# Kernel optimization log

Hardware: AMD Instinct MI355X
Metric: run time of the kernel (lower is better)

Reference implementation:

```python
import jax, jax.numpy as jnp
import numpy as np

N_NODES = 50000
N_EDGES = 625000
HIDDEN = 128
N_TYPES = 4


def setup_inputs() -> dict:
    key = jax.random.key(0)
    ks = jax.random.split(key, 10)
    s = 1.0 / np.sqrt(HIDDEN)
    return {
        "node_states": jax.random.normal(ks[0], (N_NODES, HIDDEN), dtype=jnp.float32),
        "edge_index": jax.random.randint(ks[1], (2, N_EDGES), 0, N_NODES, dtype=jnp.int64),
        "edge_type": jax.random.randint(ks[2], (N_EDGES,), 0, N_TYPES, dtype=jnp.int64),
        # per-edge-type Linear(hidden, hidden): weight [T, d, d] (torch: y = x @ W.T + b)
        "edge_W": jax.random.uniform(ks[3], (N_TYPES, HIDDEN, HIDDEN), jnp.float32, -s, s),
        "edge_b": jax.random.uniform(ks[4], (N_TYPES, HIDDEN), jnp.float32, -s, s),
        # GRUCell params (torch layout: [3d, d] for r|z|n gates)
        "w_ih": jax.random.uniform(ks[5], (3 * HIDDEN, HIDDEN), jnp.float32, -s, s),
        "w_hh": jax.random.uniform(ks[6], (3 * HIDDEN, HIDDEN), jnp.float32, -s, s),
        "b_ih": jax.random.uniform(ks[7], (3 * HIDDEN,), jnp.float32, -s, s),
        "b_hh": jax.random.uniform(ks[8], (3 * HIDDEN,), jnp.float32, -s, s),
    }


def reference(node_states, edge_index, edge_type, edge_W, edge_b, w_ih, w_hh, b_ih, b_hh):
    num_nodes = node_states.shape[0]
    src, dst = edge_index[0], edge_index[1]
    x_src = node_states[src]  # [E, d] gather of source states

    # per-edge-type linear; small fixed loop over edge types, masked accumulate
    msgs = jnp.zeros_like(x_src)
    for t in range(edge_W.shape[0]):
        m_t = x_src @ edge_W[t].T + edge_b[t]  # [E, d]
        msgs = msgs + jnp.where((edge_type == t)[:, None], m_t, 0.0)

    # scatter-sum messages into destination nodes
    agg = jax.ops.segment_sum(msgs, dst, num_segments=num_nodes)  # [N, d]

    # GRUCell(agg, node_states) — torch semantics
    gi = agg @ w_ih.T + b_ih          # [N, 3d]
    gh = node_states @ w_hh.T + b_hh  # [N, 3d]
    i_r, i_z, i_n = jnp.split(gi, 3, axis=1)
    h_r, h_z, h_n = jnp.split(gh, 3, axis=1)
    r = jax.nn.sigmoid(i_r + h_r)
    z = jax.nn.sigmoid(i_z + h_z)
    n = jnp.tanh(i_n + r * h_n)
    return (1.0 - z) * n + z * node_states
```

## Files before the change

### kernel.cpp

```cpp
#include <hip/hip_runtime.h>


typedef __attribute__((ext_vector_type(8))) short short8;
typedef __attribute__((ext_vector_type(4))) float floatx4;

#define HID 128
#define NTY 4

__device__ __forceinline__ unsigned short f2bf(float f) {
    unsigned int u = __float_as_uint(f);
    unsigned int r = (u + 0x7fffu + ((u >> 16) & 1u)) >> 16;
    return (unsigned short)r;
}
__device__ __forceinline__ float bf2f(unsigned int lo16) {
    return __uint_as_float(lo16 << 16);
}
__device__ __forceinline__ float frcp(float x) { return __builtin_amdgcn_rcpf(x); }


__global__ void prep_kernel(const float* __restrict__ h, unsigned short* __restrict__ hbf,
                            const float* __restrict__ W, unsigned short* __restrict__ Wc,
                            const float* __restrict__ w_ih, const float* __restrict__ w_hh,
                            unsigned short* __restrict__ Wg, float* __restrict__ bias4,
                            const float* __restrict__ b_ih, const float* __restrict__ b_hh,
                            int* __restrict__ deg4, int total4, int nb_cvt, int N4) {
    int b = blockIdx.x, tt = threadIdx.x;
    if (b < nb_cvt) {
        int i = b * 256 + tt;
        if (i < total4) {
            float4 v = ((const float4*)h)[i];
            uint2 o;
            o.x = (unsigned int)f2bf(v.x) | ((unsigned int)f2bf(v.y) << 16);
            o.y = (unsigned int)f2bf(v.z) | ((unsigned int)f2bf(v.w) << 16);
            ((uint2*)hbf)[i] = o;
        }
    } else if (b < nb_cvt + 256) {
        int idx = (b - nb_cvt) * 256 + tt;
        int j = idx >> 9, rem = idx & 511;
        int t = rem >> 7, k = rem & 127;
        Wc[idx] = f2bf(W[(t * HID + j) * HID + k]);
    } else if (b < nb_cvt + 768) {
        int idx = (b - nb_cvt - 256) * 256 + tt;
        int row = idx >> 8, k = idx & 255;
        int j = row >> 2, g = row & 3;
        float v = 0.0f;
        if (g == 0) v = (k < 128) ? w_ih[j * 128 + k]         : w_hh[j * 128 + (k - 128)];
        else if (g == 1) v = (k < 128) ? w_ih[(128 + j) * 128 + k] : w_hh[(128 + j) * 128 + (k - 128)];
        else if (g == 2) v = (k < 128) ? w_ih[(256 + j) * 128 + k] : 0.0f;
        else             v = (k < 128) ? 0.0f : w_hh[(256 + j) * 128 + (k - 128)];
        Wg[idx] = f2bf(v);
    } else if (b == nb_cvt + 768) {
        if (tt < 128) {
            float4 v;
            v.x = b_ih[tt] + b_hh[tt];
            v.y = b_ih[128 + tt] + b_hh[128 + tt];
            v.z = b_ih[256 + tt];
            v.w = b_hh[256 + tt];
            ((float4*)bias4)[tt] = v;
        }
    } else {
        int i = (b - nb_cvt - 769) * 256 + tt;
        if (i < N4) deg4[i] = 0;
    }
}


__global__ void hist4_kernel(const int* __restrict__ dst, const int* __restrict__ ety,
                             int* __restrict__ deg4, int E) {
    int e = blockIdx.x * blockDim.x + threadIdx.x;
    if (e < E) atomicAdd(&deg4[dst[e] * 4 + ety[e]], 1);
}

__global__ void scan_blocks4_kernel(const int* __restrict__ deg, int* __restrict__ rowptr,
                                    int* __restrict__ blocksum, int N4) {
    __shared__ int s[256];
    int t = threadIdx.x;
    int base = blockIdx.x * 1024 + t * 4;
    int v0 = 0, v1 = 0, v2 = 0, v3 = 0;
    if (base + 3 < N4) {
        v0 = deg[base]; v1 = deg[base + 1]; v2 = deg[base + 2]; v3 = deg[base + 3];
    } else {
        if (base < N4) v0 = deg[base];
        if (base + 1 < N4) v1 = deg[base + 1];
        if (base + 2 < N4) v2 = deg[base + 2];
    }
    int sum = v0 + v1 + v2 + v3;
    s[t] = sum;
    __syncthreads();
#pragma unroll
    for (int off = 1; off < 256; off <<= 1) {
        int x = (t >= off) ? s[t - off] : 0;
        __syncthreads();
        s[t] += x;
        __syncthreads();
    }
    int ex = s[t] - sum;
    if (base < N4) rowptr[base] = ex;
    if (base + 1 < N4) rowptr[base + 1] = ex + v0;
    if (base + 2 < N4) rowptr[base + 2] = ex + v0 + v1;
    if (base + 3 < N4) rowptr[base + 3] = ex + v0 + v1 + v2;
    if (t == 255) blocksum[blockIdx.x] = s[255];
}

__global__ void scan_top_kernel(const int* __restrict__ blocksum, int* __restrict__ blockoff, int nb) {
    __shared__ int s[256];
    int t = threadIdx.x;
    int v = (t < nb) ? blocksum[t] : 0;
    s[t] = v;
    __syncthreads();
#pragma unroll
    for (int off = 1; off < 256; off <<= 1) {
        int x = (t >= off) ? s[t - off] : 0;
        __syncthreads();
        s[t] += x;
        __syncthreads();
    }
    if (t < nb) blockoff[t] = s[t] - v;
}

__global__ void finalize4_kernel(int* __restrict__ rowptr, const int* __restrict__ blockoff,
                                 int* __restrict__ cursor, int N4, int E) {
    int i = blockIdx.x * blockDim.x + threadIdx.x;
    if (i >= N4) return;
    int r = rowptr[i] + blockoff[i >> 10];
    rowptr[i] = r;
    cursor[i] = r;
    if (i == 0) rowptr[N4] = E;
}

__global__ void fill4_kernel(const int* __restrict__ src, const int* __restrict__ dst,
                             const int* __restrict__ ety, int* __restrict__ cursor,
                             int* __restrict__ csr, int E) {
    int e = blockIdx.x * blockDim.x + threadIdx.x;
    if (e >= E) return;
    int pos = atomicAdd(&cursor[dst[e] * 4 + ety[e]], 1);
    csr[pos] = src[e];
}


__global__ void gather_s_kernel(const int* __restrict__ rowptr4, const int* __restrict__ csr,
                                const unsigned int* __restrict__ hbu,
                                float4* __restrict__ cnt4, unsigned int* __restrict__ Su, int N) {
    int w = blockIdx.x * (blockDim.x >> 6) + (threadIdx.x >> 6);
    if (w >= N) return;
    int lane = threadIdx.x & 63;
    int b0 = __builtin_amdgcn_readfirstlane(rowptr4[w * 4]);
    int b1 = __builtin_amdgcn_readfirstlane(rowptr4[w * 4 + 1]);
    int b2 = __builtin_amdgcn_readfirstlane(rowptr4[w * 4 + 2]);
    int b3 = __builtin_amdgcn_readfirstlane(rowptr4[w * 4 + 3]);
    int b4 = __builtin_amdgcn_readfirstlane(rowptr4[w * 4 + 4]);

    float s0 = 0.f, s1 = 0.f;
    float sn0[3], sn1[3];

    int e = b0;
    while (e + 8 <= b4) {
        int p[8];
        unsigned int u[8];
#pragma unroll
        for (int i = 0; i < 8; ++i) p[i] = csr[e + i];
#pragma unroll
        for (int i = 0; i < 8; ++i) u[i] = hbu[(size_t)p[i] * 64 + lane];
#pragma unroll
        for (int i = 0; i < 8; ++i) {
            int idx = e + i;
            if (idx == b1) { sn0[0] = s0; sn1[0] = s1; }
            if (idx == b2) { sn0[1] = s0; sn1[1] = s1; }
            if (idx == b3) { sn0[2] = s0; sn1[2] = s1; }
            s0 += bf2f(u[i] & 0xffffu);
            s1 += bf2f(u[i] >> 16);
        }
        e += 8;
    }
    {
        int rem = b4 - e;
        int p[7];
        unsigned int u[7];
#pragma unroll
        for (int i = 0; i < 7; ++i) if (i < rem) p[i] = csr[e + i];
#pragma unroll
        for (int i = 0; i < 7; ++i) if (i < rem) u[i] = hbu[(size_t)p[i] * 64 + lane];
#pragma unroll
        for (int i = 0; i < 7; ++i) {
            if (i < rem) {
                int idx = e + i;
                if (idx == b1) { sn0[0] = s0; sn1[0] = s1; }
                if (idx == b2) { sn0[1] = s0; sn1[1] = s1; }
                if (idx == b3) { sn0[2] = s0; sn1[2] = s1; }
                s0 += bf2f(u[i] & 0xffffu);
                s1 += bf2f(u[i] >> 16);
            }
        }
    }
    if (b1 == b4) { sn0[0] = s0; sn1[0] = s1; }
    if (b2 == b4) { sn0[1] = s0; sn1[1] = s1; }
    if (b3 == b4) { sn0[2] = s0; sn1[2] = s1; }

    size_t base = (size_t)w * 256 + lane;
    float a0, a1, p0 = 0.f, p1 = 0.f;
#pragma unroll
    for (int t = 0; t < 4; ++t) {
        float c0 = (t < 3) ? sn0[t] : s0;
        float c1 = (t < 3) ? sn1[t] : s1;
        a0 = c0 - p0; a1 = c1 - p1;
        p0 = c0; p1 = c1;
        Su[base + t * 64] = (unsigned int)f2bf(a0) | ((unsigned int)f2bf(a1) << 16);
    }
    if (lane == 0)
        cnt4[w] = make_float4((float)(b1 - b0), (float)(b2 - b1),
                              (float)(b3 - b2), (float)(b4 - b3));
}


__global__ __launch_bounds__(512, 4) void agg_gru(const unsigned short* __restrict__ S,
                                                  const unsigned short* __restrict__ Wc,
                                                  const unsigned short* __restrict__ Wg,
                                                  const unsigned short* __restrict__ hbf,
                                                  const float4* __restrict__ cnt4,
                                                  const float* __restrict__ eb,
                                                  const float4* __restrict__ bias4,
                                                  float* __restrict__ out, int M) {
    __shared__ __align__(16) unsigned char smem[52224];
    typedef unsigned short row136[136];
    row136* Sb0  = (row136*)smem;
    row136* Sb1  = (row136*)(smem + 17408);
    row136* Xagg = (row136*)(smem + 34816);
    float (*Outs)[132] = (float (*)[132])smem;

    const int tid = threadIdx.x;
    const int m0 = blockIdx.x * 64;
    const int lane = tid & 63, w = tid >> 6;
    const int lm = lane & 15, quad = lane >> 4;

    const int r0 = tid >> 4, sc = (tid & 15) * 8;
    const int gA = m0 + r0, gB = m0 + 32 + r0;
    const bool vA = gA < M, vB = gB < M;
    const unsigned short* SpA = S + (size_t)(vA ? gA : 0) * 512 + sc;
    const unsigned short* SpB = S + (size_t)(vB ? gB : 0) * 512 + sc;
    const uint4 Z = {0u, 0u, 0u, 0u};

    uint4 c0v = vA ? *(const uint4*)SpA : Z;
    uint4 c1v = vB ? *(const uint4*)SpB : Z;

    floatx4 accA[4];
#pragma unroll
    for (int a = 0; a < 4; ++a) accA[a] = (floatx4){0.f, 0.f, 0.f, 0.f};

#pragma unroll 1
    for (int c = 0; c < 4; ++c) {
        uint4 n0v = Z, n1v = Z;
        if (c < 3) {
            n0v = vA ? *(const uint4*)(SpA + (c + 1) * 128) : Z;
            n1v = vB ? *(const uint4*)(SpB + (c + 1) * 128) : Z;
        }
        row136* buf = (c & 1) ? Sb1 : Sb0;
        *(uint4*)&buf[r0][sc] = c0v;
        *(uint4*)&buf[32 + r0][sc] = c1v;
        __syncthreads();
#pragma unroll
        for (int ss = 0; ss < 4; ++ss) {
            short8 bw = *(const short8*)(Wc + (size_t)(w * 16 + lm) * 512 + c * 128 + ss * 32 + quad * 8);
#pragma unroll
            for (int mi = 0; mi < 4; ++mi) {
                short8 av = *(const short8*)&buf[mi * 16 + lm][ss * 32 + quad * 8];
                accA[mi] = __builtin_amdgcn_mfma_f32_16x16x32_bf16(av, bw, accA[mi], 0, 0, 0);
            }
        }
        c0v = n0v; c1v = n1v;
    }

    {
        int j = w * 16 + lm;
        float e0 = eb[j], e1 = eb[HID + j], e2 = eb[2 * HID + j], e3 = eb[3 * HID + j];
#pragma unroll
        for (int mi = 0; mi < 4; ++mi) {
#pragma unroll
            for (int r = 0; r < 4; ++r) {
                int nl = mi * 16 + quad * 4 + r;
                int gn = m0 + nl;
                if (gn >= M) gn = M - 1;
                float4 c4 = cnt4[gn];
                float v = accA[mi][r] + c4.x * e0 + c4.y * e1 + c4.z * e2 + c4.w * e3;
                Xagg[nl][j] = f2bf(v);
            }
        }
    }
    __syncthreads();

    floatx4 accB[4][4];
#pragma unroll
    for (int a = 0; a < 4; ++a)
#pragma unroll
        for (int b = 0; b < 4; ++b) accB[a][b] = (floatx4){0.f, 0.f, 0.f, 0.f};

#pragma unroll
    for (int ss = 0; ss < 8; ++ss) {
        short8 bfr[4];
#pragma unroll
        for (int ni = 0; ni < 4; ++ni) {
            if (ss < 4) {
                bfr[ni] = *(const short8*)&Xagg[ni * 16 + lm][ss * 32 + quad * 8];
            } else {
                int gr = m0 + ni * 16 + lm;
                if (gr >= M) gr = M - 1;
                bfr[ni] = *(const short8*)(hbf + (size_t)gr * HID + (ss - 4) * 32 + quad * 8);
            }
        }
        short8 af[4];
#pragma unroll
        for (int mi = 0; mi < 4; ++mi)
            af[mi] = *(const short8*)(Wg + (size_t)(w * 64 + mi * 16 + lm) * 256 + ss * 32 + quad * 8);
#pragma unroll
        for (int mi = 0; mi < 4; ++mi)
#pragma unroll
            for (int ni = 0; ni < 4; ++ni)
                accB[mi][ni] = __builtin_amdgcn_mfma_f32_16x16x32_bf16(af[mi], bfr[ni], accB[mi][ni], 0, 0, 0);
    }

#pragma unroll
    for (int mi = 0; mi < 4; ++mi) {
        int j = w * 16 + mi * 4 + quad;
        float4 bb = bias4[j];
#pragma unroll
        for (int ni = 0; ni < 4; ++ni) {
            int nl = ni * 16 + lm;
            int gn = m0 + nl;
            int gc = (gn >= M) ? (M - 1) : gn;
            float g0 = accB[mi][ni][0], g1 = accB[mi][ni][1];
            float g2 = accB[mi][ni][2], g3 = accB[mi][ni][3];
            float rr = frcp(1.f + __expf(-(g0 + bb.x)));
            float zz = frcp(1.f + __expf(-(g1 + bb.y)));
            float aa = g2 + bb.z + rr * (g3 + bb.w);
            float nn = 1.f - 2.f * frcp(1.f + __expf(2.f * aa));
            float hv = bf2f((unsigned int)hbf[(size_t)gc * HID + j]);
            Outs[nl][j] = nn + zz * (hv - nn);
        }
    }
    __syncthreads();

    {
        int row = tid >> 3;
        int cb = (tid & 7) * 16;
        int node = m0 + row;
        if (node < M) {
            float* dstp = out + (size_t)node * HID + cb;
#pragma unroll
            for (int i = 0; i < 4; ++i)
                *(float4*)(dstp + i * 4) = *(const float4*)&Outs[row][cb + i * 4];
        }
    }
}


extern "C" void kernel_launch(void* const* d_in, const int* in_sizes, int n_in,
                              void* d_out, int out_size, void* d_ws, size_t ws_size,
                              hipStream_t stream) {
    const float* node_states = (const float*)d_in[0];
    const int*   edge_index  = (const int*)d_in[1];
    const int*   edge_type   = (const int*)d_in[2];
    const float* edge_W      = (const float*)d_in[3];
    const float* edge_b      = (const float*)d_in[4];
    const float* w_ih        = (const float*)d_in[5];
    const float* w_hh        = (const float*)d_in[6];
    const float* b_ih        = (const float*)d_in[7];
    const float* b_hh        = (const float*)d_in[8];

    const int M = in_sizes[0] / HID;
    const int E = in_sizes[1] / 2;
    const int N4 = M * 4;
    const int* src = edge_index;
    const int* dst = edge_index + E;

    char* ws = (char*)d_ws;
    size_t off = 0;
    unsigned short* hbf   = (unsigned short*)(ws + off); off += (size_t)M * HID * 2;
    float*          bias4 = (float*)(ws + off);          off += (size_t)128 * 4 * 4;
    unsigned short* S     = (unsigned short*)(ws + off); off += (size_t)M * 512 * 2;
    unsigned short* Wcat  = (unsigned short*)(ws + off); off += (size_t)128 * 512 * 2;
    unsigned short* Wgru  = (unsigned short*)(ws + off); off += (size_t)512 * 256 * 2;
    float*          cnt4  = (float*)(ws + off);          off += (size_t)M * 4 * 4;
    int* deg4     = (int*)(ws + off); off += (size_t)N4 * 4;
    int* rowptr4  = (int*)(ws + off); off += (size_t)(N4 + 1) * 4;
    int* cursor4  = (int*)(ws + off); off += (size_t)N4 * 4;
    int* blocksum = (int*)(ws + off); off += 256 * 4;
    int* blockoff = (int*)(ws + off); off += 256 * 4;
    int* csr      = (int*)(ws + off); off += (size_t)E * 4;

    const int total4 = M * HID / 4;
    const int nb_cvt = (total4 + 255) / 256;
    const int nb_zero = (N4 + 255) / 256;
    const int nb_scan = (N4 + 1023) / 1024;

    prep_kernel<<<nb_cvt + 769 + nb_zero, 256, 0, stream>>>(
        node_states, hbf, edge_W, Wcat, w_ih, w_hh, Wgru, bias4, b_ih, b_hh,
        deg4, total4, nb_cvt, N4);

    hist4_kernel<<<(E + 255) / 256, 256, 0, stream>>>(dst, edge_type, deg4, E);
    scan_blocks4_kernel<<<nb_scan, 256, 0, stream>>>(deg4, rowptr4, blocksum, N4);
    scan_top_kernel<<<1, 256, 0, stream>>>(blocksum, blockoff, nb_scan);
    finalize4_kernel<<<(N4 + 255) / 256, 256, 0, stream>>>(rowptr4, blockoff, cursor4, N4, E);
    fill4_kernel<<<(E + 255) / 256, 256, 0, stream>>>(src, dst, edge_type, cursor4, csr, E);

    gather_s_kernel<<<(M + 3) / 4, 256, 0, stream>>>(rowptr4, csr, (const unsigned int*)hbf,
                                                     (float4*)cnt4, (unsigned int*)S, M);

    agg_gru<<<(M + 63) / 64, 512, 0, stream>>>(S, Wcat, Wgru, hbf, (const float4*)cnt4,
                                               edge_b, (const float4*)bias4, (float*)d_out, M);
}
```

Before: 273.6 us.

## Fuse CSR build and gather into one cooperative kernel; shrink GRU tile to 32 nodes

Seven preprocessing launches (convert, histogram, two-level scan, finalize, fill, gather) are merged into a single cooperative persistent kernel of 768 blocks, with grid.sync between phases. This removes per-launch overhead and the gaps between launches. The GRU kernel is retiled from 64 nodes and 512 threads to 32 nodes and 256 threads, with half the shared memory, and computes its gate outputs in two halves. The grid barriers add their own cost, the fixed grid size may underfill phases with a lot of work, and smaller tiles reload weights more often.

```diff
diff --git a/kernel.cpp b/kernel.cpp
--- a/kernel.cpp
+++ b/kernel.cpp
@@ -1,4 +1,7 @@
 #include <hip/hip_runtime.h>
+#include <hip/hip_cooperative_groups.h>
+
+namespace cg = cooperative_groups;
 
 
 typedef __attribute__((ext_vector_type(8))) short short8;
@@ -18,171 +21,144 @@
 __device__ __forceinline__ float frcp(float x) { return __builtin_amdgcn_rcpf(x); }
 
 
-__global__ void prep_kernel(const float* __restrict__ h, unsigned short* __restrict__ hbf,
-                            const float* __restrict__ W, unsigned short* __restrict__ Wc,
-                            const float* __restrict__ w_ih, const float* __restrict__ w_hh,
-                            unsigned short* __restrict__ Wg, float* __restrict__ bias4,
-                            const float* __restrict__ b_ih, const float* __restrict__ b_hh,
-                            int* __restrict__ deg4, int total4, int nb_cvt, int N4) {
-    int b = blockIdx.x, tt = threadIdx.x;
-    if (b < nb_cvt) {
-        int i = b * 256 + tt;
-        if (i < total4) {
-            float4 v = ((const float4*)h)[i];
-            uint2 o;
-            o.x = (unsigned int)f2bf(v.x) | ((unsigned int)f2bf(v.y) << 16);
-            o.y = (unsigned int)f2bf(v.z) | ((unsigned int)f2bf(v.w) << 16);
-            ((uint2*)hbf)[i] = o;
-        }
-    } else if (b < nb_cvt + 256) {
-        int idx = (b - nb_cvt) * 256 + tt;
+struct BuildArgs {
+    const float* h; unsigned short* hbf;
+    const float* W; unsigned short* Wc;
+    const float* wih; const float* whh; unsigned short* Wg;
+    float* bias4; const float* bih; const float* bhh;
+    int* deg4; int* rowptr4; int* cursor4; int* blocksum; int* blockoff; int* csr;
+    const int* src; const int* dst; const int* ety;
+    float4* cnt4; unsigned int* Su;
+    int M, E, N4, total4;
+};
+
+__global__ __launch_bounds__(256, 4) void build_kernel(BuildArgs a) {
+    cg::grid_group grid = cg::this_grid();
+    __shared__ int s[256];
+    const int t = threadIdx.x;
+    const int gtid = blockIdx.x * 256 + t;
+    const int nth = gridDim.x * 256;
+
+    for (int i = gtid; i < a.total4; i += nth) {
+        float4 v = ((const float4*)a.h)[i];
+        uint2 o;
+        o.x = (unsigned int)f2bf(v.x) | ((unsigned int)f2bf(v.y) << 16);
+        o.y = (unsigned int)f2bf(v.z) | ((unsigned int)f2bf(v.w) << 16);
+        ((uint2*)a.hbf)[i] = o;
+    }
+    for (int idx = gtid; idx < 128 * 512; idx += nth) {
         int j = idx >> 9, rem = idx & 511;
-        int t = rem >> 7, k = rem & 127;
-        Wc[idx] = f2bf(W[(t * HID + j) * HID + k]);
-    } else if (b < nb_cvt + 768) {
-        int idx = (b - nb_cvt - 256) * 256 + tt;
+        int ty = rem >> 7, k = rem & 127;
+        a.Wc[idx] = f2bf(a.W[(ty * HID + j) * HID + k]);
+    }
+    for (int idx = gtid; idx < 512 * 256; idx += nth) {
         int row = idx >> 8, k = idx & 255;
         int j = row >> 2, g = row & 3;
         float v = 0.0f;
-        if (g == 0) v = (k < 128) ? w_ih[j * 128 + k]         : w_hh[j * 128 + (k - 128)];
-        else if (g == 1) v = (k < 128) ? w_ih[(128 + j) * 128 + k] : w_hh[(128 + j) * 128 + (k - 128)];
-        else if (g == 2) v = (k < 128) ? w_ih[(256 + j) * 128 + k] : 0.0f;
-        else             v = (k < 128) ? 0.0f : w_hh[(256 + j) * 128 + (k - 128)];
-        Wg[idx] = f2bf(v);
-    } else if (b == nb_cvt + 768) {
-        if (tt < 128) {
-            float4 v;
-            v.x = b_ih[tt] + b_hh[tt];
-            v.y = b_ih[128 + tt] + b_hh[128 + tt];
-            v.z = b_ih[256 + tt];
-            v.w = b_hh[256 + tt];
-            ((float4*)bias4)[tt] = v;
-        }
-    } else {
-        int i = (b - nb_cvt - 769) * 256 + tt;
-        if (i < N4) deg4[i] = 0;
-    }
-}
-
-
-__global__ void hist4_kernel(const int* __restrict__ dst, const int* __restrict__ ety,
-                             int* __restrict__ deg4, int E) {
-    int e = blockIdx.x * blockDim.x + threadIdx.x;
-    if (e < E) atomicAdd(&deg4[dst[e] * 4 + ety[e]], 1);
-}
-
-__global__ void scan_blocks4_kernel(const int* __restrict__ deg, int* __restrict__ rowptr,
-                                    int* __restrict__ blocksum, int N4) {
-    __shared__ int s[256];
-    int t = threadIdx.x;
-    int base = blockIdx.x * 1024 + t * 4;
-    int v0 = 0, v1 = 0, v2 = 0, v3 = 0;
-    if (base + 3 < N4) {
-        v0 = deg[base]; v1 = deg[base + 1]; v2 = deg[base + 2]; v3 = deg[base + 3];
-    } else {
-        if (base < N4) v0 = deg[base];
-        if (base + 1 < N4) v1 = deg[base + 1];
-        if (base + 2 < N4) v2 = deg[base + 2];
-    }
-    int sum = v0 + v1 + v2 + v3;
-    s[t] = sum;
-    __syncthreads();
-#pragma unroll
-    for (int off = 1; off < 256; off <<= 1) {
-        int x = (t >= off) ? s[t - off] : 0;
-        __syncthreads();
-        s[t] += x;
-        __syncthreads();
-    }
-    int ex = s[t] - sum;
-    if (base < N4) rowptr[base] = ex;
-    if (base + 1 < N4) rowptr[base + 1] = ex + v0;
-    if (base + 2 < N4) rowptr[base + 2] = ex + v0 + v1;
-    if (base + 3 < N4) rowptr[base + 3] = ex + v0 + v1 + v2;
-    if (t == 255) blocksum[blockIdx.x] = s[255];
-}
-
-__global__ void scan_top_kernel(const int* __restrict__ blocksum, int* __restrict__ blockoff, int nb) {
-    __shared__ int s[256];
-    int t = threadIdx.x;
-    int v = (t < nb) ? blocksum[t] : 0;
-    s[t] = v;
-    __syncthreads();
-#pragma unroll
-    for (int off = 1; off < 256; off <<= 1) {
-        int x = (t >= off) ? s[t - off] : 0;
-        __syncthreads();
-        s[t] += x;
-        __syncthreads();
-    }
-    if (t < nb) blockoff[t] = s[t] - v;
-}
-
-__global__ void finalize4_kernel(int* __restrict__ rowptr, const int* __restrict__ blockoff,
-                                 int* __restrict__ cursor, int N4, int E) {
-    int i = blockIdx.x * blockDim.x + threadIdx.x;
-    if (i >= N4) return;
-    int r = rowptr[i] + blockoff[i >> 10];
-    rowptr[i] = r;
-    cursor[i] = r;
-    if (i == 0) rowptr[N4] = E;
-}
-
-__global__ void fill4_kernel(const int* __restrict__ src, const int* __restrict__ dst,
-                             const int* __restrict__ ety, int* __restrict__ cursor,
-                             int* __restrict__ csr, int E) {
-    int e = blockIdx.x * blockDim.x + threadIdx.x;
-    if (e >= E) return;
-    int pos = atomicAdd(&cursor[dst[e] * 4 + ety[e]], 1);
-    csr[pos] = src[e];
-}
-
-
-__global__ void gather_s_kernel(const int* __restrict__ rowptr4, const int* __restrict__ csr,
-                                const unsigned int* __restrict__ hbu,
-                                float4* __restrict__ cnt4, unsigned int* __restrict__ Su, int N) {
-    int w = blockIdx.x * (blockDim.x >> 6) + (threadIdx.x >> 6);
-    if (w >= N) return;
-    int lane = threadIdx.x & 63;
-    int b0 = __builtin_amdgcn_readfirstlane(rowptr4[w * 4]);
-    int b1 = __builtin_amdgcn_readfirstlane(rowptr4[w * 4 + 1]);
-    int b2 = __builtin_amdgcn_readfirstlane(rowptr4[w * 4 + 2]);
-    int b3 = __builtin_amdgcn_readfirstlane(rowptr4[w * 4 + 3]);
-    int b4 = __builtin_amdgcn_readfirstlane(rowptr4[w * 4 + 4]);
-
-    float s0 = 0.f, s1 = 0.f;
-    float sn0[3], sn1[3];
-
-    int e = b0;
-    while (e + 8 <= b4) {
-        int p[8];
-        unsigned int u[8];
-#pragma unroll
-        for (int i = 0; i < 8; ++i) p[i] = csr[e + i];
-#pragma unroll
-        for (int i = 0; i < 8; ++i) u[i] = hbu[(size_t)p[i] * 64 + lane];
-#pragma unroll
-        for (int i = 0; i < 8; ++i) {
-            int idx = e + i;
-            if (idx == b1) { sn0[0] = s0; sn1[0] = s1; }
-            if (idx == b2) { sn0[1] = s0; sn1[1] = s1; }
-            if (idx == b3) { sn0[2] = s0; sn1[2] = s1; }
-            s0 += bf2f(u[i] & 0xffffu);
-            s1 += bf2f(u[i] >> 16);
-        }
-        e += 8;
-    }
-    {
-        int rem = b4 - e;
-        int p[7];
-        unsigned int u[7];
-#pragma unroll
-        for (int i = 0; i < 7; ++i) if (i < rem) p[i] = csr[e + i];
-#pragma unroll
-        for (int i = 0; i < 7; ++i) if (i < rem) u[i] = hbu[(size_t)p[i] * 64 + lane];
-#pragma unroll
-        for (int i = 0; i < 7; ++i) {
-            if (i < rem) {
+        if (g == 0)      v = (k < 128) ? a.wih[j * 128 + k]         : a.whh[j * 128 + (k - 128)];
+        else if (g == 1) v = (k < 128) ? a.wih[(128 + j) * 128 + k] : a.whh[(128 + j) * 128 + (k - 128)];
+        else if (g == 2) v = (k < 128) ? a.wih[(256 + j) * 128 + k] : 0.0f;
+        else             v = (k < 128) ? 0.0f : a.whh[(256 + j) * 128 + (k - 128)];
+        a.Wg[idx] = f2bf(v);
+    }
+    if (gtid < 128) {
+        float4 v;
+        v.x = a.bih[gtid] + a.bhh[gtid];
+        v.y = a.bih[128 + gtid] + a.bhh[128 + gtid];
+        v.z = a.bih[256 + gtid];
+        v.w = a.bhh[256 + gtid];
+        ((float4*)a.bias4)[gtid] = v;
+    }
+    for (int i = gtid; i < a.N4; i += nth) a.deg4[i] = 0;
+    grid.sync();
+
+    for (int e = gtid; e < a.E; e += nth)
+        atomicAdd(&a.deg4[a.dst[e] * 4 + a.ety[e]], 1);
+    grid.sync();
+
+    const int nbscan = (a.N4 + 1023) >> 10;
+    for (int vb = blockIdx.x; vb < nbscan; vb += gridDim.x) {
+        int base = vb * 1024 + t * 4;
+        int v0 = 0, v1 = 0, v2 = 0, v3 = 0;
+        if (base + 3 < a.N4) {
+            v0 = a.deg4[base]; v1 = a.deg4[base + 1]; v2 = a.deg4[base + 2]; v3 = a.deg4[base + 3];
+        } else {
+            if (base < a.N4) v0 = a.deg4[base];
+            if (base + 1 < a.N4) v1 = a.deg4[base + 1];
+            if (base + 2 < a.N4) v2 = a.deg4[base + 2];
+        }
+        int sum = v0 + v1 + v2 + v3;
+        s[t] = sum;
+        __syncthreads();
+#pragma unroll
+        for (int off = 1; off < 256; off <<= 1) {
+            int x = (t >= off) ? s[t - off] : 0;
+            __syncthreads();
+            s[t] += x;
+            __syncthreads();
+        }
+        int ex = s[t] - sum;
+        if (base < a.N4) a.rowptr4[base] = ex;
+        if (base + 1 < a.N4) a.rowptr4[base + 1] = ex + v0;
+        if (base + 2 < a.N4) a.rowptr4[base + 2] = ex + v0 + v1;
+        if (base + 3 < a.N4) a.rowptr4[base + 3] = ex + v0 + v1 + v2;
+        if (t == 255) a.blocksum[vb] = s[255];
+        __syncthreads();
+    }
+    grid.sync();
+
+    if (blockIdx.x == 0) {
+        int v = (t < nbscan) ? a.blocksum[t] : 0;
+        s[t] = v;
+        __syncthreads();
+#pragma unroll
+        for (int off = 1; off < 256; off <<= 1) {
+            int x = (t >= off) ? s[t - off] : 0;
+            __syncthreads();
+            s[t] += x;
+            __syncthreads();
+        }
+        if (t < nbscan) a.blockoff[t] = s[t] - v;
+    }
+    grid.sync();
+
+    for (int i = gtid; i < a.N4; i += nth) {
+        int r = a.rowptr4[i] + a.blockoff[i >> 10];
+        a.rowptr4[i] = r;
+        a.cursor4[i] = r;
+    }
+    if (gtid == 0) a.rowptr4[a.N4] = a.E;
+    grid.sync();
+
+    for (int e = gtid; e < a.E; e += nth) {
+        int pos = atomicAdd(&a.cursor4[a.dst[e] * 4 + a.ety[e]], 1);
+        a.csr[pos] = a.src[e];
+    }
+    grid.sync();
+
+    const int lane = t & 63;
+    const int gw = gtid >> 6, nwav = nth >> 6;
+    for (int nd = gw; nd < a.M; nd += nwav) {
+        int b0 = __builtin_amdgcn_readfirstlane(a.rowptr4[nd * 4]);
+        int b1 = __builtin_amdgcn_readfirstlane(a.rowptr4[nd * 4 + 1]);
+        int b2 = __builtin_amdgcn_readfirstlane(a.rowptr4[nd * 4 + 2]);
+        int b3 = __builtin_amdgcn_readfirstlane(a.rowptr4[nd * 4 + 3]);
+        int b4 = __builtin_amdgcn_readfirstlane(a.rowptr4[nd * 4 + 4]);
+
+        float s0 = 0.f, s1 = 0.f;
+        float sn0[3], sn1[3];
+        const unsigned int* hbu = a.Su ? (const unsigned int*)a.hbf : (const unsigned int*)a.hbf;
+
+        int e = b0;
+        while (e + 8 <= b4) {
+            int p[8];
+            unsigned int u[8];
+#pragma unroll
+            for (int i = 0; i < 8; ++i) p[i] = a.csr[e + i];
+#pragma unroll
+            for (int i = 0; i < 8; ++i) u[i] = hbu[(size_t)p[i] * 64 + lane];
+#pragma unroll
+            for (int i = 0; i < 8; ++i) {
                 int idx = e + i;
                 if (idx == b1) { sn0[0] = s0; sn1[0] = s1; }
                 if (idx == b2) { sn0[1] = s0; sn1[1] = s1; }
@@ -190,29 +166,50 @@
                 s0 += bf2f(u[i] & 0xffffu);
                 s1 += bf2f(u[i] >> 16);
             }
-        }
-    }
-    if (b1 == b4) { sn0[0] = s0; sn1[0] = s1; }
-    if (b2 == b4) { sn0[1] = s0; sn1[1] = s1; }
-    if (b3 == b4) { sn0[2] = s0; sn1[2] = s1; }
-
-    size_t base = (size_t)w * 256 + lane;
-    float a0, a1, p0 = 0.f, p1 = 0.f;
-#pragma unroll
-    for (int t = 0; t < 4; ++t) {
-        float c0 = (t < 3) ? sn0[t] : s0;
-        float c1 = (t < 3) ? sn1[t] : s1;
-        a0 = c0 - p0; a1 = c1 - p1;
-        p0 = c0; p1 = c1;
-        Su[base + t * 64] = (unsigned int)f2bf(a0) | ((unsigned int)f2bf(a1) << 16);
-    }
-    if (lane == 0)
-        cnt4[w] = make_float4((float)(b1 - b0), (float)(b2 - b1),
-                              (float)(b3 - b2), (float)(b4 - b3));
+            e += 8;
+        }
+        {
+            int rem = b4 - e;
+            int p[7];
+            unsigned int u[7];
+#pragma unroll
+            for (int i = 0; i < 7; ++i) if (i < rem) p[i] = a.csr[e + i];
+#pragma unroll
+            for (int i = 0; i < 7; ++i) if (i < rem) u[i] = hbu[(size_t)p[i] * 64 + lane];
+#pragma unroll
+            for (int i = 0; i < 7; ++i) {
+                if (i < rem) {
+                    int idx = e + i;
+                    if (idx == b1) { sn0[0] = s0; sn1[0] = s1; }
+                    if (idx == b2) { sn0[1] = s0; sn1[1] = s1; }
+                    if (idx == b3) { sn0[2] = s0; sn1[2] = s1; }
+                    s0 += bf2f(u[i] & 0xffffu);
+                    s1 += bf2f(u[i] >> 16);
+                }
+            }
+        }
+        if (b1 == b4) { sn0[0] = s0; sn1[0] = s1; }
+        if (b2 == b4) { sn0[1] = s0; sn1[1] = s1; }
+        if (b3 == b4) { sn0[2] = s0; sn1[2] = s1; }
+
+        size_t base = (size_t)nd * 256 + lane;
+        float p0 = 0.f, p1 = 0.f;
+#pragma unroll
+        for (int ty = 0; ty < 4; ++ty) {
+            float c0 = (ty < 3) ? sn0[ty] : s0;
+            float c1 = (ty < 3) ? sn1[ty] : s1;
+            float a0 = c0 - p0, a1 = c1 - p1;
+            p0 = c0; p1 = c1;
+            a.Su[base + ty * 64] = (unsigned int)f2bf(a0) | ((unsigned int)f2bf(a1) << 16);
+        }
+        if (lane == 0)
+            a.cnt4[nd] = make_float4((float)(b1 - b0), (float)(b2 - b1),
+                                     (float)(b3 - b2), (float)(b4 - b3));
+    }
 }
 
 
-__global__ __launch_bounds__(512, 4) void agg_gru(const unsigned short* __restrict__ S,
+__global__ __launch_bounds__(256, 5) void agg_gru(const unsigned short* __restrict__ S,
                                                   const unsigned short* __restrict__ Wc,
                                                   const unsigned short* __restrict__ Wg,
                                                   const unsigned short* __restrict__ hbf,
@@ -220,20 +217,20 @@
                                                   const float* __restrict__ eb,
                                                   const float4* __restrict__ bias4,
                                                   float* __restrict__ out, int M) {
-    __shared__ __align__(16) unsigned char smem[52224];
+    __shared__ __align__(16) unsigned char smem[26112];
     typedef unsigned short row136[136];
     row136* Sb0  = (row136*)smem;
-    row136* Sb1  = (row136*)(smem + 17408);
-    row136* Xagg = (row136*)(smem + 34816);
-    float (*Outs)[132] = (float (*)[132])smem;
+    row136* Sb1  = (row136*)(smem + 8704);
+    row136* Xagg = (row136*)(smem + 17408);
+    float (*Outs)[68] = (float (*)[68])smem;
 
     const int tid = threadIdx.x;
-    const int m0 = blockIdx.x * 64;
+    const int m0 = blockIdx.x * 32;
     const int lane = tid & 63, w = tid >> 6;
     const int lm = lane & 15, quad = lane >> 4;
 
     const int r0 = tid >> 4, sc = (tid & 15) * 8;
-    const int gA = m0 + r0, gB = m0 + 32 + r0;
+    const int gA = m0 + r0, gB = m0 + 16 + r0;
     const bool vA = gA < M, vB = gB < M;
     const unsigned short* SpA = S + (size_t)(vA ? gA : 0) * 512 + sc;
     const unsigned short* SpB = S + (size_t)(vB ? gB : 0) * 512 + sc;
@@ -242,9 +239,11 @@
     uint4 c0v = vA ? *(const uint4*)SpA : Z;
     uint4 c1v = vB ? *(const uint4*)SpB : Z;
 
-    floatx4 accA[4];
-#pragma unroll
-    for (int a = 0; a < 4; ++a) accA[a] = (floatx4){0.f, 0.f, 0.f, 0.f};
+    floatx4 accA[2][2];
+#pragma unroll
+    for (int x = 0; x < 2; ++x)
+#pragma unroll
+        for (int y = 0; y < 2; ++y) accA[x][y] = (floatx4){0.f, 0.f, 0.f, 0.f};
 
 #pragma unroll 1
     for (int c = 0; c < 4; ++c) {
@@ -255,99 +254,102 @@
         }
         row136* buf = (c & 1) ? Sb1 : Sb0;
         *(uint4*)&buf[r0][sc] = c0v;
-        *(uint4*)&buf[32 + r0][sc] = c1v;
+        *(uint4*)&buf[16 + r0][sc] = c1v;
         __syncthreads();
 #pragma unroll
         for (int ss = 0; ss < 4; ++ss) {
-            short8 bw = *(const short8*)(Wc + (size_t)(w * 16 + lm) * 512 + c * 128 + ss * 32 + quad * 8);
-#pragma unroll
-            for (int mi = 0; mi < 4; ++mi) {
-                short8 av = *(const short8*)&buf[mi * 16 + lm][ss * 32 + quad * 8];
-                accA[mi] = __builtin_amdgcn_mfma_f32_16x16x32_bf16(av, bw, accA[mi], 0, 0, 0);
+            short8 av0 = *(const short8*)&buf[lm][ss * 32 + quad * 8];
+            short8 av1 = *(const short8*)&buf[16 + lm][ss * 32 + quad * 8];
+#pragma unroll
+            for (int ni = 0; ni < 2; ++ni) {
+                short8 bw = *(const short8*)(Wc + (size_t)(w * 32 + ni * 16 + lm) * 512 + c * 128 + ss * 32 + quad * 8);
+                accA[0][ni] = __builtin_amdgcn_mfma_f32_16x16x32_bf16(av0, bw, accA[0][ni], 0, 0, 0);
+                accA[1][ni] = __builtin_amdgcn_mfma_f32_16x16x32_bf16(av1, bw, accA[1][ni], 0, 0, 0);
             }
         }
         c0v = n0v; c1v = n1v;
     }
 
-    {
-        int j = w * 16 + lm;
+#pragma unroll
+    for (int ni = 0; ni < 2; ++ni) {
+        int j = w * 32 + ni * 16 + lm;
         float e0 = eb[j], e1 = eb[HID + j], e2 = eb[2 * HID + j], e3 = eb[3 * HID + j];
 #pragma unroll
-        for (int mi = 0; mi < 4; ++mi) {
+        for (int mi = 0; mi < 2; ++mi) {
 #pragma unroll
             for (int r = 0; r < 4; ++r) {
                 int nl = mi * 16 + quad * 4 + r;
                 int gn = m0 + nl;
                 if (gn >= M) gn = M - 1;
                 float4 c4 = cnt4[gn];
-                float v = accA[mi][r] + c4.x * e0 + c4.y * e1 + c4.z * e2 + c4.w * e3;
+                float v = accA[mi][ni][r] + c4.x * e0 + c4.y * e1 + c4.z * e2 + c4.w * e3;
                 Xagg[nl][j] = f2bf(v);
             }
         }
     }
     __syncthreads();
 
-    floatx4 accB[4][4];
-#pragma unroll
-    for (int a = 0; a < 4; ++a)
-#pragma unroll
-        for (int b = 0; b < 4; ++b) accB[a][b] = (floatx4){0.f, 0.f, 0.f, 0.f};
-
-#pragma unroll
-    for (int ss = 0; ss < 8; ++ss) {
-        short8 bfr[4];
-#pragma unroll
-        for (int ni = 0; ni < 4; ++ni) {
-            if (ss < 4) {
-                bfr[ni] = *(const short8*)&Xagg[ni * 16 + lm][ss * 32 + quad * 8];
-            } else {
-                int gr = m0 + ni * 16 + lm;
-                if (gr >= M) gr = M - 1;
-                bfr[ni] = *(const short8*)(hbf + (size_t)gr * HID + (ss - 4) * 32 + quad * 8);
-            }
-        }
-        short8 af[4];
-#pragma unroll
-        for (int mi = 0; mi < 4; ++mi)
-            af[mi] = *(const short8*)(Wg + (size_t)(w * 64 + mi * 16 + lm) * 256 + ss * 32 + quad * 8);
-#pragma unroll
-        for (int mi = 0; mi < 4; ++mi)
-#pragma unroll
-            for (int ni = 0; ni < 4; ++ni)
-                accB[mi][ni] = __builtin_amdgcn_mfma_f32_16x16x32_bf16(af[mi], bfr[ni], accB[mi][ni], 0, 0, 0);
-    }
-
-#pragma unroll
-    for (int mi = 0; mi < 4; ++mi) {
-        int j = w * 16 + mi * 4 + quad;
-        float4 bb = bias4[j];
-#pragma unroll
-        for (int ni = 0; ni < 4; ++ni) {
-            int nl = ni * 16 + lm;
-            int gn = m0 + nl;
-            int gc = (gn >= M) ? (M - 1) : gn;
-            float g0 = accB[mi][ni][0], g1 = accB[mi][ni][1];
-            float g2 = accB[mi][ni][2], g3 = accB[mi][ni][3];
-            float rr = frcp(1.f + __expf(-(g0 + bb.x)));
-            float zz = frcp(1.f + __expf(-(g1 + bb.y)));
-            float aa = g2 + bb.z + rr * (g3 + bb.w);
-            float nn = 1.f - 2.f * frcp(1.f + __expf(2.f * aa));
-            float hv = bf2f((unsigned int)hbf[(size_t)gc * HID + j]);
-            Outs[nl][j] = nn + zz * (hv - nn);
-        }
-    }
-    __syncthreads();
-
-    {
-        int row = tid >> 3;
-        int cb = (tid & 7) * 16;
-        int node = m0 + row;
-        if (node < M) {
-            float* dstp = out + (size_t)node * HID + cb;
-#pragma unroll
-            for (int i = 0; i < 4; ++i)
-                *(float4*)(dstp + i * 4) = *(const float4*)&Outs[row][cb + i * 4];
-        }
+#pragma unroll 1
+    for (int h = 0; h < 2; ++h) {
+        floatx4 accB[4][2];
+#pragma unroll
+        for (int x = 0; x < 4; ++x)
+#pragma unroll
+            for (int y = 0; y < 2; ++y) accB[x][y] = (floatx4){0.f, 0.f, 0.f, 0.f};
+
+#pragma unroll
+        for (int ss = 0; ss < 8; ++ss) {
+            short8 bfr[2];
+#pragma unroll
+            for (int ni = 0; ni < 2; ++ni) {
+                if (ss < 4) {
+                    bfr[ni] = *(const short8*)&Xagg[ni * 16 + lm][ss * 32 + quad * 8];
+                } else {
+                    int gr = m0 + ni * 16 + lm;
+                    if (gr >= M) gr = M - 1;
+                    bfr[ni] = *(const short8*)(hbf + (size_t)gr * HID + (ss - 4) * 32 + quad * 8);
+                }
+            }
+#pragma unroll
+            for (int mi = 0; mi < 4; ++mi) {
+                short8 af = *(const short8*)(Wg + (size_t)(h * 256 + w * 64 + mi * 16 + lm) * 256 + ss * 32 + quad * 8);
+                accB[mi][0] = __builtin_amdgcn_mfma_f32_16x16x32_bf16(af, bfr[0], accB[mi][0], 0, 0, 0);
+                accB[mi][1] = __builtin_amdgcn_mfma_f32_16x16x32_bf16(af, bfr[1], accB[mi][1], 0, 0, 0);
+            }
+        }
+
+#pragma unroll
+        for (int mi = 0; mi < 4; ++mi) {
+            int j = h * 64 + w * 16 + mi * 4 + quad;
+            float4 bb = bias4[j];
+#pragma unroll
+            for (int ni = 0; ni < 2; ++ni) {
+                int nl = ni * 16 + lm;
+                int gn = m0 + nl;
+                int gc = (gn >= M) ? (M - 1) : gn;
+                float g0 = accB[mi][ni][0], g1 = accB[mi][ni][1];
+                float g2 = accB[mi][ni][2], g3 = accB[mi][ni][3];
+                float rr = frcp(1.f + __expf(-(g0 + bb.x)));
+                float zz = frcp(1.f + __expf(-(g1 + bb.y)));
+                float aa = g2 + bb.z + rr * (g3 + bb.w);
+                float nn = 1.f - 2.f * frcp(1.f + __expf(2.f * aa));
+                float hv = bf2f((unsigned int)hbf[(size_t)gc * HID + j]);
+                Outs[nl][j - h * 64] = nn + zz * (hv - nn);
+            }
+        }
+        __syncthreads();
+
+        {
+            int row = tid >> 3;
+            int cb = (tid & 7) * 8;
+            int node = m0 + row;
+            if (node < M) {
+                float* dstp = out + (size_t)node * HID + h * 64 + cb;
+                *(float4*)(dstp)     = *(const float4*)&Outs[row][cb];
+                *(float4*)(dstp + 4) = *(const float4*)&Outs[row][cb + 4];
+            }
+        }
+        __syncthreads();
     }
 }
 
@@ -387,23 +389,22 @@
     int* csr      = (int*)(ws + off); off += (size_t)E * 4;
 
     const int total4 = M * HID / 4;
-    const int nb_cvt = (total4 + 255) / 256;
-    const int nb_zero = (N4 + 255) / 256;
-    const int nb_scan = (N4 + 1023) / 1024;
-
-    prep_kernel<<<nb_cvt + 769 + nb_zero, 256, 0, stream>>>(
-        node_states, hbf, edge_W, Wcat, w_ih, w_hh, Wgru, bias4, b_ih, b_hh,
-        deg4, total4, nb_cvt, N4);
-
-    hist4_kernel<<<(E + 255) / 256, 256, 0, stream>>>(dst, edge_type, deg4, E);
-    scan_blocks4_kernel<<<nb_scan, 256, 0, stream>>>(deg4, rowptr4, blocksum, N4);
-    scan_top_kernel<<<1, 256, 0, stream>>>(blocksum, blockoff, nb_scan);
-    finalize4_kernel<<<(N4 + 255) / 256, 256, 0, stream>>>(rowptr4, blockoff, cursor4, N4, E);
-    fill4_kernel<<<(E + 255) / 256, 256, 0, stream>>>(src, dst, edge_type, cursor4, csr, E);
-
-    gather_s_kernel<<<(M + 3) / 4, 256, 0, stream>>>(rowptr4, csr, (const unsigned int*)hbf,
-                                                     (float4*)cnt4, (unsigned int*)S, M);
-
-    agg_gru<<<(M + 63) / 64, 512, 0, stream>>>(S, Wcat, Wgru, hbf, (const float4*)cnt4,
+
+    BuildArgs ba;
+    ba.h = node_states; ba.hbf = hbf;
+    ba.W = edge_W; ba.Wc = Wcat;
+    ba.wih = w_ih; ba.whh = w_hh; ba.Wg = Wgru;
+    ba.bias4 = bias4; ba.bih = b_ih; ba.bhh = b_hh;
+    ba.deg4 = deg4; ba.rowptr4 = rowptr4; ba.cursor4 = cursor4;
+    ba.blocksum = blocksum; ba.blockoff = blockoff; ba.csr = csr;
+    ba.src = src; ba.dst = dst; ba.ety = edge_type;
+    ba.cnt4 = (float4*)cnt4; ba.Su = (unsigned int*)S;
+    ba.M = M; ba.E = E; ba.N4 = N4; ba.total4 = total4;
+
+    void* params[] = {&ba};
+    hipLaunchCooperativeKernel((void*)build_kernel, dim3(768), dim3(256),
+                               params, 0, stream);
+
+    agg_gru<<<(M + 31) / 32, 256, 0, stream>>>(S, Wcat, Wgru, hbf, (const float4*)cnt4,
                                                edge_b, (const float4*)bias4, (float*)d_out, M);
 }
```

New measurement: 882.0 us. 222% more time.

## Stage weight tiles in XOR-swizzled LDS and split GRU GEMM into gate chunks

Applied to the files above, without the earlier changes.

The agg_gru kernel now copies the message-weight and GRU-weight tiles from global memory into shared memory and reads MFMA operands from there. Previously each wave loaded its operands straight from global memory. All LDS tiles switch from padded rows to an XOR swizzle to avoid bank conflicts. The GRU GEMM is split into four gate-column chunks with a two-step K loop, which cuts the accumulator registers from sixteen to four vectors. In exchange it adds more __syncthreads barriers and removes the prefetch double-buffering of S, so global loads are no longer overlapped with compute.

```diff
diff --git a/kernel.cpp b/kernel.cpp
--- a/kernel.cpp
+++ b/kernel.cpp
@@ -220,27 +220,19 @@
                                                   const float* __restrict__ eb,
                                                   const float4* __restrict__ bias4,
                                                   float* __restrict__ out, int M) {
-    __shared__ __align__(16) unsigned char smem[52224];
-    typedef unsigned short row136[136];
-    row136* Sb0  = (row136*)smem;
-    row136* Sb1  = (row136*)(smem + 17408);
-    row136* Xagg = (row136*)(smem + 34816);
-    float (*Outs)[132] = (float (*)[132])smem;
+    __shared__ __align__(16) unsigned short Sreg[64 * 128];
+    __shared__ __align__(16) unsigned short Wreg[128 * 128];
+    __shared__ __align__(16) unsigned short Xagg[64 * 128];
+    float* OutsF = (float*)Wreg;
 
     const int tid = threadIdx.x;
     const int m0 = blockIdx.x * 64;
     const int lane = tid & 63, w = tid >> 6;
     const int lm = lane & 15, quad = lane >> 4;
-
-    const int r0 = tid >> 4, sc = (tid & 15) * 8;
-    const int gA = m0 + r0, gB = m0 + 32 + r0;
-    const bool vA = gA < M, vB = gB < M;
-    const unsigned short* SpA = S + (size_t)(vA ? gA : 0) * 512 + sc;
-    const unsigned short* SpB = S + (size_t)(vB ? gB : 0) * 512 + sc;
     const uint4 Z = {0u, 0u, 0u, 0u};
 
-    uint4 c0v = vA ? *(const uint4*)SpA : Z;
-    uint4 c1v = vB ? *(const uint4*)SpB : Z;
+    const int sr = tid >> 4;
+    const int sg = tid & 15;
 
     floatx4 accA[4];
 #pragma unroll
@@ -248,30 +240,37 @@
 
 #pragma unroll 1
     for (int c = 0; c < 4; ++c) {
-        uint4 n0v = Z, n1v = Z;
-        if (c < 3) {
-            n0v = vA ? *(const uint4*)(SpA + (c + 1) * 128) : Z;
-            n1v = vB ? *(const uint4*)(SpB + (c + 1) * 128) : Z;
-        }
-        row136* buf = (c & 1) ? Sb1 : Sb0;
-        *(uint4*)&buf[r0][sc] = c0v;
-        *(uint4*)&buf[32 + r0][sc] = c1v;
+        {
+            int gA = m0 + sr, gB = m0 + 32 + sr;
+            uint4 vA = (gA < M) ? *(const uint4*)(S + (size_t)gA * 512 + c * 128 + sg * 8) : Z;
+            uint4 vB = (gB < M) ? *(const uint4*)(S + (size_t)gB * 512 + c * 128 + sg * 8) : Z;
+            *(uint4*)&Sreg[sr * 128 + ((sg ^ (sr & 7)) << 3)] = vA;
+            *(uint4*)&Sreg[(32 + sr) * 128 + ((sg ^ (sr & 7)) << 3)] = vB;
+        }
+#pragma unroll
+        for (int p = 0; p < 4; ++p) {
+            int j = p * 32 + sr;
+            uint4 v = *(const uint4*)(Wc + (size_t)j * 512 + c * 128 + sg * 8);
+            *(uint4*)&Wreg[j * 128 + ((sg ^ (j & 7)) << 3)] = v;
+        }
         __syncthreads();
 #pragma unroll
         for (int ss = 0; ss < 4; ++ss) {
-            short8 bw = *(const short8*)(Wc + (size_t)(w * 16 + lm) * 512 + c * 128 + ss * 32 + quad * 8);
+            int g = ss * 4 + quad;
+            short8 bw = *(const short8*)&Wreg[(w * 16 + lm) * 128 + ((g ^ (lm & 7)) << 3)];
 #pragma unroll
             for (int mi = 0; mi < 4; ++mi) {
-                short8 av = *(const short8*)&buf[mi * 16 + lm][ss * 32 + quad * 8];
+                short8 av = *(const short8*)&Sreg[(mi * 16 + lm) * 128 + ((g ^ (lm & 7)) << 3)];
                 accA[mi] = __builtin_amdgcn_mfma_f32_16x16x32_bf16(av, bw, accA[mi], 0, 0, 0);
             }
         }
-        c0v = n0v; c1v = n1v;
+        __syncthreads();
     }
 
     {
         int j = w * 16 + lm;
         float e0 = eb[j], e1 = eb[HID + j], e2 = eb[2 * HID + j], e3 = eb[3 * HID + j];
+        int jg = j >> 3, jr = j & 7;
 #pragma unroll
         for (int mi = 0; mi < 4; ++mi) {
 #pragma unroll
@@ -281,59 +280,80 @@
                 if (gn >= M) gn = M - 1;
                 float4 c4 = cnt4[gn];
                 float v = accA[mi][r] + c4.x * e0 + c4.y * e1 + c4.z * e2 + c4.w * e3;
-                Xagg[nl][j] = f2bf(v);
+                Xagg[nl * 128 + ((jg ^ (nl & 7)) << 3) + jr] = f2bf(v);
             }
         }
     }
     __syncthreads();
 
-    floatx4 accB[4][4];
-#pragma unroll
-    for (int a = 0; a < 4; ++a)
-#pragma unroll
-        for (int b = 0; b < 4; ++b) accB[a][b] = (floatx4){0.f, 0.f, 0.f, 0.f};
-
-#pragma unroll
-    for (int ss = 0; ss < 8; ++ss) {
-        short8 bfr[4];
-#pragma unroll
-        for (int ni = 0; ni < 4; ++ni) {
-            if (ss < 4) {
-                bfr[ni] = *(const short8*)&Xagg[ni * 16 + lm][ss * 32 + quad * 8];
-            } else {
-                int gr = m0 + ni * 16 + lm;
-                if (gr >= M) gr = M - 1;
-                bfr[ni] = *(const short8*)(hbf + (size_t)gr * HID + (ss - 4) * 32 + quad * 8);
-            }
-        }
-        short8 af[4];
-#pragma unroll
-        for (int mi = 0; mi < 4; ++mi)
-            af[mi] = *(const short8*)(Wg + (size_t)(w * 64 + mi * 16 + lm) * 256 + ss * 32 + quad * 8);
-#pragma unroll
-        for (int mi = 0; mi < 4; ++mi)
-#pragma unroll
-            for (int ni = 0; ni < 4; ++ni)
-                accB[mi][ni] = __builtin_amdgcn_mfma_f32_16x16x32_bf16(af[mi], bfr[ni], accB[mi][ni], 0, 0, 0);
-    }
-
-#pragma unroll
-    for (int mi = 0; mi < 4; ++mi) {
-        int j = w * 16 + mi * 4 + quad;
-        float4 bb = bias4[j];
+    {
+        int gA = m0 + sr, gB = m0 + 32 + sr;
+        uint4 vA = (gA < M) ? *(const uint4*)(hbf + (size_t)gA * HID + sg * 8) : Z;
+        uint4 vB = (gB < M) ? *(const uint4*)(hbf + (size_t)gB * HID + sg * 8) : Z;
+        *(uint4*)&Sreg[sr * 128 + ((sg ^ (sr & 7)) << 3)] = vA;
+        *(uint4*)&Sreg[(32 + sr) * 128 + ((sg ^ (sr & 7)) << 3)] = vB;
+    }
+
+    float fin[4][4];
+
+#pragma unroll 1
+    for (int gc = 0; gc < 4; ++gc) {
+        floatx4 accB[4];
+#pragma unroll
+        for (int a = 0; a < 4; ++a) accB[a] = (floatx4){0.f, 0.f, 0.f, 0.f};
+
+#pragma unroll 1
+        for (int kc = 0; kc < 2; ++kc) {
+#pragma unroll
+            for (int p = 0; p < 4; ++p) {
+                int rr = p * 32 + sr;
+                int grow = gc * 128 + rr;
+                uint4 v = *(const uint4*)(Wg + (size_t)grow * 256 + kc * 128 + sg * 8);
+                *(uint4*)&Wreg[rr * 128 + ((sg ^ (rr & 7)) << 3)] = v;
+            }
+            __syncthreads();
+#pragma unroll
+            for (int ss = 0; ss < 4; ++ss) {
+                int g = ss * 4 + quad;
+                short8 af = *(const short8*)&Wreg[(w * 16 + lm) * 128 + ((g ^ (lm & 7)) << 3)];
+#pragma unroll
+                for (int ni = 0; ni < 4; ++ni) {
+                    const unsigned short* bsrc = kc ? Sreg : Xagg;
+                    short8 bfr = *(const short8*)&bsrc[(ni * 16 + lm) * 128 + ((g ^ (lm & 7)) << 3)];
+                    accB[ni] = __builtin_amdgcn_mfma_f32_16x16x32_bf16(af, bfr, accB[ni], 0, 0, 0);
+                }
+            }
+            __syncthreads();
+        }
+
+        {
+            int j = gc * 32 + w * 4 + quad;
+            float4 bb = bias4[j];
+            int jg = j >> 3, jr = j & 7;
+#pragma unroll
+            for (int ni = 0; ni < 4; ++ni) {
+                int nl = ni * 16 + lm;
+                float g0 = accB[ni][0], g1 = accB[ni][1];
+                float g2 = accB[ni][2], g3 = accB[ni][3];
+                float rr = frcp(1.f + __expf(-(g0 + bb.x)));
+                float zz = frcp(1.f + __expf(-(g1 + bb.y)));
+                float aa = g2 + bb.z + rr * (g3 + bb.w);
+                float nn = 1.f - 2.f * frcp(1.f + __expf(2.f * aa));
+                float hv = bf2f((unsigned int)Sreg[nl * 128 + ((jg ^ (nl & 7)) << 3) + jr]);
+                fin[gc][ni] = nn + zz * (hv - nn);
+            }
+        }
+    }
+    __syncthreads();
+
+#pragma unroll
+    for (int gc = 0; gc < 4; ++gc) {
+        int j = gc * 32 + w * 4 + quad;
+        int gq = j >> 2, jr = j & 3;
 #pragma unroll
         for (int ni = 0; ni < 4; ++ni) {
             int nl = ni * 16 + lm;
-            int gn = m0 + nl;
-            int gc = (gn >= M) ? (M - 1) : gn;
-            float g0 = accB[mi][ni][0], g1 = accB[mi][ni][1];
-            float g2 = accB[mi][ni][2], g3 = accB[mi][ni][3];
-            float rr = frcp(1.f + __expf(-(g0 + bb.x)));
-            float zz = frcp(1.f + __expf(-(g1 + bb.y)));
-            float aa = g2 + bb.z + rr * (g3 + bb.w);
-            float nn = 1.f - 2.f * frcp(1.f + __expf(2.f * aa));
-            float hv = bf2f((unsigned int)hbf[(size_t)gc * HID + j]);
-            Outs[nl][j] = nn + zz * (hv - nn);
+            OutsF[nl * 128 + ((gq ^ (nl & 7)) << 2) + jr] = fin[gc][ni];
         }
     }
     __syncthreads();
@@ -345,8 +365,10 @@
         if (node < M) {
             float* dstp = out + (size_t)node * HID + cb;
 #pragma unroll
-            for (int i = 0; i < 4; ++i)
-                *(float4*)(dstp + i * 4) = *(const float4*)&Outs[row][cb + i * 4];
+            for (int i = 0; i < 4; ++i) {
+                int gq = (cb >> 2) + i;
+                *(float4*)(dstp + i * 4) = *(const float4*)&OutsF[row * 128 + ((gq ^ (row & 7)) << 2)];
+            }
         }
     }
 }
```

Measured after the change: 244.6 us. -10.6%, faster.
